# Kernel tuning notes

Measured on AMD Instinct MI355X. Metric: run time of the kernel, lower is better.

The kernel has to match this reference:

```python
import jax, jax.numpy as jnp
import numpy as np

EPS = 1e-15


def setup_inputs() -> dict:
    key = jax.random.key(0)
    ks = jax.random.split(key, 10)
    F, B, L = 10, 16384, 20          # num_field, batch, hist_len
    V, D = 1000000, 16               # sparse_feature_number, sparse_feature_dim
    FEAT, E, S, G, T = 160, 8, 64, 3, 32  # feature_size, expert_num, expert_size, gate_num, tower_size
    return {
        "ids": jax.random.randint(ks[0], (F, B, L), 0, V, dtype=jnp.int64),
        "emb_table": jax.random.uniform(ks[1], (V, D), jnp.float32, -1.0, 1.0),
        "expert_w": jax.random.normal(ks[2], (E, FEAT, S), jnp.float32) * 0.05,
        "expert_b": jnp.full((E, S), 0.1, jnp.float32),
        "gate_w": jax.random.normal(ks[3], (G, FEAT, E), jnp.float32) * 0.05,
        "gate_b": jnp.full((G, E), 0.1, jnp.float32),
        "tower_w": jax.random.normal(ks[4], (G, S, T), jnp.float32) * 0.05,
        "tower_b": jnp.full((G, T), 0.1, jnp.float32),
        "out_w": jax.random.normal(ks[5], (G, T, 2), jnp.float32) * 0.05,
        "out_b": jnp.full((G, 2), 0.1, jnp.float32),
    }


def reference(ids, emb_table, expert_w, expert_b, gate_w, gate_b,
              tower_w, tower_b, out_w, out_b):
    # Embedding lookup + sum over history: [F,B,L,D] -> [F,B,D]
    field_emb = emb_table[ids].sum(axis=2)
    B = field_emb.shape[1]
    # concat per-field embeddings along feature axis: [B, F*D]
    x = jnp.transpose(field_emb, (1, 0, 2)).reshape(B, -1)
    # all experts as one batched GEMM: [B,E,S]
    experts = jax.nn.relu(jnp.einsum('bf,efs->bes', x, expert_w) + expert_b)
    # gate softmax over experts: [B,G,E]
    gates = jax.nn.softmax(jnp.einsum('bf,gfe->bge', x, gate_w) + gate_b, axis=-1)
    # gate-weighted expert mixture: [B,G,S]
    mix = jnp.einsum('bge,bes->bgs', gates, experts)
    # towers: [B,G,T] -> logits [B,G,2]
    tow = jax.nn.relu(jnp.einsum('bgs,gst->bgt', mix, tower_w) + tower_b)
    logits = jnp.einsum('bgt,gto->bgo', tow, out_w) + out_b
    probs = jnp.clip(jax.nn.softmax(logits, axis=-1), EPS, 1.0 - EPS)  # [B,3,2]
    ctr, cvr, imp = probs[:, 0], probs[:, 1], probs[:, 2]
    ctr1 = ctr[:, 1:2]
    cvr1 = cvr[:, 1:2]
    ctcvr1 = ctr1 * cvr1
    ctcvr = jnp.concatenate([1.0 - ctcvr1, ctcvr1], axis=1)
    imp1 = imp[:, 1:2]
    # out_list packed along last axis: ctr(2), ctr1(1), cvr(2), cvr1(1), ctcvr(2), ctcvr1(1), imp1(1) -> [B,10]
    return jnp.concatenate([ctr, ctr1, cvr, cvr1, ctcvr, ctcvr1, imp1], axis=1)
```

## Files before the change

### kernel.cpp

```cpp
#include <hip/hip_runtime.h>
#include <hip/hip_bf16.h>
#include <cstdint>
#include <cstddef>

#define NFIELD 10
#define BATCH  16384
#define NIDS   20
#define DEMB   16
#define NFEAT  160
#define NEXP   8
#define NS     64
#define NG     3
#define NT     32

#define XB        ((size_t)BATCH * NFEAT * 2)
#define BP_OFF_B  XB
#define BM_OFF_B  (BP_OFF_B + 174080)
#define BT_OFF_B  (BM_OFF_B + 2176)
#define TB2_OFF_B (BT_OFF_B + 12288)
#define OWF_OFF_B (TB2_OFF_B + 384)
#define OBF_OFF_B (OWF_OFF_B + 768)
#define FLG_OFF_B (OBF_OFF_B + 32)

typedef short bfrag __attribute__((ext_vector_type(8)));
typedef float f32x4 __attribute__((ext_vector_type(4)));

__device__ __forceinline__ float bflo(uint32_t u) {
    union { uint32_t u; float f; } c; c.u = u << 16; return c.f;
}
__device__ __forceinline__ float bfhi(uint32_t u) {
    union { uint32_t u; float f; } c; c.u = u & 0xffff0000u; return c.f;
}
__device__ __forceinline__ float bf1(uint16_t v) {
    union { uint32_t u; float f; } c; c.u = ((uint32_t)v) << 16; return c.f;
}
__device__ __forceinline__ uint16_t f2bf(float f) {
    union { float f; uint32_t u; } c; c.f = f;
    uint32_t r = c.u + 0x7fffu + ((c.u >> 16) & 1u);
    return (uint16_t)(r >> 16);
}
__device__ __forceinline__ float ldw(const void* p, int i, bool bf) {
    return bf ? bf1(((const uint16_t*)p)[i]) : ((const float*)p)[i];
}
__device__ __forceinline__ uint16_t ldb16(const void* p, int i, bool bf) {
    return bf ? ((const uint16_t*)p)[i] : f2bf(((const float*)p)[i]);
}

__global__ __launch_bounds__(64) void sniff_dtypes(
    const uint32_t* __restrict__ ids_w,
    const uint32_t* __restrict__ emb_w,
    int* __restrict__ flags)
{
    int t = threadIdx.x;
    size_t p = (size_t)t * 25000;
    uint32_t hi = ids_w[2 * p + 1];
    int n_hi = __popcll(__ballot(hi != 0));

    size_t q = (size_t)t * 125000;
    uint32_t w = emb_w[q];
    uint32_t v = (w >> 8) & 0x7Fu;
    int n_bf = __popcll(__ballot(v >= 0x3Bu && v <= 0x3Fu));

    if (t == 0) {
        flags[0] = (n_hi < 8)   ? 1 : 0;
        flags[1] = (n_bf >= 32) ? 1 : 0;
    }
}

__global__ __launch_bounds__(256) void pack_weights(
    const void* __restrict__ ew, const void* __restrict__ eb,
    const void* __restrict__ gw, const void* __restrict__ gb,
    const void* __restrict__ tw, const void* __restrict__ tb,
    const void* __restrict__ ow, const void* __restrict__ ob,
    uint16_t* __restrict__ bp, float* __restrict__ bm,
    uint16_t* __restrict__ bt, float* __restrict__ tb2,
    float* __restrict__ owf, float* __restrict__ obf,
    const int* __restrict__ flags)
{
    const bool bf = flags[1] != 0;
    int i = blockIdx.x * 256 + threadIdx.x;
    if (i < 10880) {
        int nt = i / 320, rem = i % 320;
        int ks = rem / 64, l = rem % 64;
        int n  = nt * 16 + (l & 15);
        int kb = ks * 32 + ((l >> 4) * 8);
        uint16_t v[8];
        #pragma unroll
        for (int j = 0; j < 8; ++j) {
            int k = kb + j;
            uint16_t x;
            if (n < 512)      x = ldb16(ew, (n >> 6) * 10240 + k * 64 + (n & 63), bf);
            else if (n < 536) x = ldb16(gw, ((n - 512) >> 3) * 1280 + k * 8 + ((n - 512) & 7), bf);
            else              x = 0;
            v[j] = x;
        }
        uint4 o;
        o.x = (uint32_t)v[0] | ((uint32_t)v[1] << 16);
        o.y = (uint32_t)v[2] | ((uint32_t)v[3] << 16);
        o.z = (uint32_t)v[4] | ((uint32_t)v[5] << 16);
        o.w = (uint32_t)v[6] | ((uint32_t)v[7] << 16);
        ((uint4*)bp)[i] = o;
    } else if (i < 11648) {
        int it = i - 10880;
        int g = it / 256, rem = it % 256;
        int ntile = rem / 128, ks = (rem / 64) & 1, l = rem % 64;
        int t  = ntile * 16 + (l & 15);
        int sb = ks * 32 + ((l >> 4) * 8);
        uint16_t v[8];
        #pragma unroll
        for (int j = 0; j < 8; ++j)
            v[j] = ldb16(tw, g * 2048 + (sb + j) * 32 + t, bf);
        uint4 o;
        o.x = (uint32_t)v[0] | ((uint32_t)v[1] << 16);
        o.y = (uint32_t)v[2] | ((uint32_t)v[3] << 16);
        o.z = (uint32_t)v[4] | ((uint32_t)v[5] << 16);
        o.w = (uint32_t)v[6] | ((uint32_t)v[7] << 16);
        ((uint4*)bt)[it] = o;
    } else if (i < 12192) {
        int n = i - 11648;
        bm[n] = (n < 512) ? ldw(eb, n, bf) : (n < 536 ? ldw(gb, n - 512, bf) : 0.0f);
    } else if (i < 12288) {
        int n = i - 12192; tb2[n] = ldw(tb, n, bf);
    } else if (i < 12480) {
        int n = i - 12288; owf[n] = ldw(ow, n, bf);
    } else if (i < 12486) {
        int n = i - 12480; obf[n] = ldw(ob, n, bf);
    }
}

__global__ __launch_bounds__(256) void gather_sum(
    const void* __restrict__ ids_raw,
    const void* __restrict__ emb_raw,
    uint16_t* __restrict__ xout,
    const int* __restrict__ flags)
{
    const bool i64 = flags[0] != 0;
    const bool bf  = flags[1] != 0;
    int tid = blockIdx.x * 256 + threadIdx.x;
    int f = tid >> 14;
    int b = tid & (BATCH - 1);

    int idv[NIDS];
    if (i64) {
        const int4* p4 = (const int4*)((const long long*)ids_raw +
                                       ((size_t)f * BATCH + b) * NIDS);
        #pragma unroll
        for (int j = 0; j < NIDS / 2; ++j) {
            int4 q = p4[j];
            idv[2 * j + 0] = q.x;
            idv[2 * j + 1] = q.z;
        }
    } else {
        const int4* p4 = (const int4*)((const int*)ids_raw +
                                       ((size_t)f * BATCH + b) * NIDS);
        #pragma unroll
        for (int j = 0; j < NIDS / 4; ++j) {
            int4 q = p4[j];
            idv[4 * j + 0] = q.x; idv[4 * j + 1] = q.y;
            idv[4 * j + 2] = q.z; idv[4 * j + 3] = q.w;
        }
    }

    float acc[16];
    #pragma unroll
    for (int d = 0; d < 16; ++d) acc[d] = 0.0f;

    if (bf) {
        #pragma unroll 5
        for (int l = 0; l < NIDS; ++l) {
            const uint4* row = (const uint4*)((const uint16_t*)emb_raw +
                                              (size_t)idv[l] * DEMB);
            uint4 r0 = row[0];
            uint4 r1 = row[1];
            acc[0]  += bflo(r0.x); acc[1]  += bfhi(r0.x);
            acc[2]  += bflo(r0.y); acc[3]  += bfhi(r0.y);
            acc[4]  += bflo(r0.z); acc[5]  += bfhi(r0.z);
            acc[6]  += bflo(r0.w); acc[7]  += bfhi(r0.w);
            acc[8]  += bflo(r1.x); acc[9]  += bfhi(r1.x);
            acc[10] += bflo(r1.y); acc[11] += bfhi(r1.y);
            acc[12] += bflo(r1.z); acc[13] += bfhi(r1.z);
            acc[14] += bflo(r1.w); acc[15] += bfhi(r1.w);
        }
    } else {
        #pragma unroll 5
        for (int l = 0; l < NIDS; ++l) {
            const float4* row = (const float4*)((const float*)emb_raw +
                                                (size_t)idv[l] * DEMB);
            float4 r0 = row[0], r1 = row[1], r2 = row[2], r3 = row[3];
            acc[0]  += r0.x; acc[1]  += r0.y; acc[2]  += r0.z; acc[3]  += r0.w;
            acc[4]  += r1.x; acc[5]  += r1.y; acc[6]  += r1.z; acc[7]  += r1.w;
            acc[8]  += r2.x; acc[9]  += r2.y; acc[10] += r2.z; acc[11] += r2.w;
            acc[12] += r3.x; acc[13] += r3.y; acc[14] += r3.z; acc[15] += r3.w;
        }
    }

    uint32_t p[8];
    #pragma unroll
    for (int j = 0; j < 8; ++j)
        p[j] = (uint32_t)f2bf(acc[2 * j]) | ((uint32_t)f2bf(acc[2 * j + 1]) << 16);

    uint4* dst = (uint4*)(xout + (size_t)b * NFEAT + f * DEMB);
    dst[0] = make_uint4(p[0], p[1], p[2], p[3]);
    dst[1] = make_uint4(p[4], p[5], p[6], p[7]);
}

__global__ __launch_bounds__(256) void moe_fwd(
    const uint16_t* __restrict__ xbf,
    const uint16_t* __restrict__ bp,
    const float*    __restrict__ bm,
    const uint16_t* __restrict__ btw,
    const float*    __restrict__ btb,
    const float*    __restrict__ owf,
    const float*    __restrict__ obf,
    const void* __restrict__ ew,
    const void* __restrict__ eb,
    const void* __restrict__ gw,
    const void* __restrict__ gb,
    const void* __restrict__ tw,
    const void* __restrict__ tb,
    const int* __restrict__ flags,
    void* __restrict__ out)
{
    __shared__ uint16_t exp_lds[32][520];
    __shared__ float    gate_lds[32][33];
    __shared__ uint16_t mix_lds[32][200];
    __shared__ float    tow_lds[32][100];
    __shared__ float    prob_lds[32][6];
    __shared__ int      badf, badt;

    const bool bfw = flags[1] != 0;
    const int tid = threadIdx.x;
    const int w = tid >> 6, l = tid & 63;
    const int lm = l & 15, q = l >> 4;
    const int b0 = blockIdx.x * 32;
    const int mrow = (w & 1) * 16;
    const int nhalf = w >> 1;

    if (tid == 0) { badf = 0; badt = 0; }

    bfrag a[5];
    {
        const uint16_t* xr = xbf + (size_t)(b0 + mrow + lm) * NFEAT + q * 8;
        #pragma unroll
        for (int ks = 0; ks < 5; ++ks)
            a[ks] = *(const bfrag*)(xr + ks * 32);
    }

    const int nt0 = nhalf * 17;
    for (int it = 0; it < 17; ++it) {
        int nt = nt0 + it;
        f32x4 acc = {0.0f, 0.0f, 0.0f, 0.0f};
        const bfrag* bpp = (const bfrag*)bp + (size_t)(nt * 5) * 64 + l;
        #pragma unroll
        for (int ks = 0; ks < 5; ++ks) {
            bfrag b = bpp[ks * 64];
            acc = __builtin_amdgcn_mfma_f32_16x16x32_bf16(a[ks], b, acc, 0, 0, 0);
        }
        int col = nt * 16 + lm;
        float bias = bm[col];
        if (col < 512) {
            #pragma unroll
            for (int r = 0; r < 4; ++r)
                exp_lds[mrow + q * 4 + r][col] = f2bf(fmaxf(acc[r] + bias, 0.0f));
        } else {
            #pragma unroll
            for (int r = 0; r < 4; ++r)
                gate_lds[mrow + q * 4 + r][col - 512] = acc[r] + bias;
        }
    }
    __syncthreads();

    if (tid < 64) {
        int s = tid & 31;
        int c = (tid * 67) & 511;
        int e = c >> 6, ss = c & 63;
        const uint16_t* xr = xbf + (size_t)(b0 + s) * NFEAT;
        float acal = ldw(eb, c, bfw);
        for (int k = 0; k < NFEAT; ++k)
            acal = fmaf(bf1(xr[k]), ldw(ew, e * 10240 + k * 64 + ss, bfw), acal);
        float want = fmaxf(acal, 0.0f);
        float got  = bf1(exp_lds[s][c]);
        if (fabsf(want - got) > 0.06f + 0.01f * fabsf(want)) badf = 1;
    } else if (tid < 88) {
        int idx = tid - 64;
        int s   = (tid * 5) & 31;
        int g = idx >> 3, e = idx & 7;
        const uint16_t* xr = xbf + (size_t)(b0 + s) * NFEAT;
        float acal = ldw(gb, idx, bfw);
        for (int k = 0; k < NFEAT; ++k)
            acal = fmaf(bf1(xr[k]), ldw(gw, g * 1280 + k * 8 + e, bfw), acal);
        if (fabsf(acal - gate_lds[s][idx]) > 0.04f + 0.01f * fabsf(acal)) badf = 1;
    }
    __syncthreads();

    if (badf) {
        uint16_t* xs = &mix_lds[0][0];
        for (int i = tid; i < 32 * NFEAT; i += 256) {
            int s = i / NFEAT, k = i - s * NFEAT;
            xs[s * 200 + k] = xbf[(size_t)(b0 + s) * NFEAT + k];
        }
        __syncthreads();
        int s2 = tid >> 3, j2 = tid & 7;
        for (int c = j2; c < 512; c += 8) {
            int e = c >> 6, ss = c & 63;
            float acal = ldw(eb, c, bfw);
            #pragma unroll 4
            for (int k = 0; k < NFEAT; ++k)
                acal = fmaf(bf1(xs[s2 * 200 + k]), ldw(ew, e * 10240 + k * 64 + ss, bfw), acal);
            exp_lds[s2][c] = f2bf(fmaxf(acal, 0.0f));
        }
        if (j2 < 3) {
            int g = j2;
            for (int e = 0; e < 8; ++e) {
                float acal = ldw(gb, g * 8 + e, bfw);
                #pragma unroll 4
                for (int k = 0; k < NFEAT; ++k)
                    acal = fmaf(bf1(xs[s2 * 200 + k]), ldw(gw, g * 1280 + k * 8 + e, bfw), acal);
                gate_lds[s2][g * 8 + e] = acal;
            }
        }
        __syncthreads();
    }

    const int sm = tid >> 3, j = tid & 7;

    if (j < 3) {
        float* gl = &gate_lds[sm][j * 8];
        float m = gl[0];
        #pragma unroll
        for (int e = 1; e < 8; ++e) m = fmaxf(m, gl[e]);
        float ex[8], s = 0.0f;
        #pragma unroll
        for (int e = 0; e < 8; ++e) { ex[e] = __expf(gl[e] - m); s += ex[e]; }
        float inv = 1.0f / s;
        #pragma unroll
        for (int e = 0; e < 8; ++e) gl[e] = ex[e] * inv;
    }
    __syncthreads();

    for (int g = 0; g < NG; ++g) {
        float m8[8];
        #pragma unroll
        for (int i = 0; i < 8; ++i) m8[i] = 0.0f;
        #pragma unroll
        for (int e = 0; e < NEXP; ++e) {
            float gv = gate_lds[sm][g * 8 + e];
            uint4 u = *(const uint4*)&exp_lds[sm][e * 64 + j * 8];
            m8[0] = fmaf(gv, bflo(u.x), m8[0]); m8[1] = fmaf(gv, bfhi(u.x), m8[1]);
            m8[2] = fmaf(gv, bflo(u.y), m8[2]); m8[3] = fmaf(gv, bfhi(u.y), m8[3]);
            m8[4] = fmaf(gv, bflo(u.z), m8[4]); m8[5] = fmaf(gv, bfhi(u.z), m8[5]);
            m8[6] = fmaf(gv, bflo(u.w), m8[6]); m8[7] = fmaf(gv, bfhi(u.w), m8[7]);
        }
        uint4 o;
        o.x = (uint32_t)f2bf(m8[0]) | ((uint32_t)f2bf(m8[1]) << 16);
        o.y = (uint32_t)f2bf(m8[2]) | ((uint32_t)f2bf(m8[3]) << 16);
        o.z = (uint32_t)f2bf(m8[4]) | ((uint32_t)f2bf(m8[5]) << 16);
        o.w = (uint32_t)f2bf(m8[6]) | ((uint32_t)f2bf(m8[7]) << 16);
        *(uint4*)&mix_lds[sm][g * 64 + j * 8] = o;
    }
    __syncthreads();

    for (int u = w; u < 12; u += 4) {
        int g = u >> 2, mt = (u >> 1) & 1, ntile = u & 1;
        f32x4 acc = {0.0f, 0.0f, 0.0f, 0.0f};
        #pragma unroll
        for (int ks = 0; ks < 2; ++ks) {
            bfrag av = *(const bfrag*)&mix_lds[mt * 16 + lm][g * 64 + ks * 32 + q * 8];
            bfrag bv = *(const bfrag*)(btw + (size_t)((((g * 2 + ntile) * 2 + ks) * 64 + l)) * 8);
            acc = __builtin_amdgcn_mfma_f32_16x16x32_bf16(av, bv, acc, 0, 0, 0);
        }
        int t = ntile * 16 + lm;
        float bias = btb[g * 32 + t];
        #pragma unroll
        for (int r = 0; r < 4; ++r)
            tow_lds[mt * 16 + q * 4 + r][g * 32 + t] = fmaxf(acc[r] + bias, 0.0f);
    }
    __syncthreads();

    if (tid < 64) {
        int s   = tid & 31;
        int idx = (tid * 29) % 96;
        int g = idx >> 5, t = idx & 31;
        float acal = ldw(tb, g * 32 + t, bfw);
        for (int ss = 0; ss < NS; ++ss)
            acal = fmaf(bf1(mix_lds[s][g * 64 + ss]), ldw(tw, g * 2048 + ss * 32 + t, bfw), acal);
        float want = fmaxf(acal, 0.0f);
        if (fabsf(want - tow_lds[s][g * 32 + t]) > 0.04f + 0.01f * fabsf(want)) badt = 1;
    }
    __syncthreads();

    if (badt) {
        int s2 = tid >> 3, j2 = tid & 7;
        for (int idx = j2; idx < 96; idx += 8) {
            int g = idx >> 5, t = idx & 31;
            float acal = ldw(tb, g * 32 + t, bfw);
            #pragma unroll 4
            for (int ss = 0; ss < NS; ++ss)
                acal = fmaf(bf1(mix_lds[s2][g * 64 + ss]), ldw(tw, g * 2048 + ss * 32 + t, bfw), acal);
            tow_lds[s2][g * 32 + t] = fmaxf(acal, 0.0f);
        }
        __syncthreads();
    }

    if (j < 3) {
        int g = j;
        float l0 = obf[2 * g], l1 = obf[2 * g + 1];
        #pragma unroll 8
        for (int t = 0; t < NT; ++t) {
            float tv = tow_lds[sm][g * 32 + t];
            l0 = fmaf(tv, owf[g * 64 + 2 * t], l0);
            l1 = fmaf(tv, owf[g * 64 + 2 * t + 1], l1);
        }
        float m  = fmaxf(l0, l1);
        float e0 = __expf(l0 - m);
        float e1 = __expf(l1 - m);
        float inv = 1.0f / (e0 + e1);
        float p0 = fminf(fmaxf(e0 * inv, 1e-15f), 1.0f);
        float p1 = fminf(fmaxf(e1 * inv, 1e-15f), 1.0f);
        prob_lds[sm][2 * g + 0] = p0;
        prob_lds[sm][2 * g + 1] = p1;
    }
    __syncthreads();

    {
        float ctr0 = prob_lds[sm][0], ctr1 = prob_lds[sm][1];
        float cvr0 = prob_lds[sm][2], cvr1 = prob_lds[sm][3];
        float imp1 = prob_lds[sm][5];
        float ctcvr1 = ctr1 * cvr1;
        for (int o = j; o < 10; o += 8) {
            float v;
            switch (o) {
                case 0: v = ctr0; break;
                case 1: v = ctr1; break;
                case 2: v = ctr1; break;
                case 3: v = cvr0; break;
                case 4: v = cvr1; break;
                case 5: v = cvr1; break;
                case 6: v = 1.0f - ctcvr1; break;
                case 7: v = ctcvr1; break;
                case 8: v = ctcvr1; break;
                default: v = imp1; break;
            }
            if (bfw) ((uint16_t*)out)[(size_t)(b0 + sm) * 10 + o] = f2bf(v);
            else     ((float*)out)[(size_t)(b0 + sm) * 10 + o]    = v;
        }
    }
}

extern "C" void kernel_launch(void* const* d_in, const int* in_sizes, int n_in,
                              void* d_out, int out_size, void* d_ws, size_t ws_size,
                              hipStream_t stream) {
    const void* ids = d_in[0];
    const void* emb = d_in[1];

    char* ws = (char*)d_ws;
    uint16_t* xbf = (uint16_t*)ws;
    uint16_t* bpk = (uint16_t*)(ws + BP_OFF_B);
    float*    bm  = (float*)(ws + BM_OFF_B);
    uint16_t* btw = (uint16_t*)(ws + BT_OFF_B);
    float*    tb2 = (float*)(ws + TB2_OFF_B);
    float*    owf = (float*)(ws + OWF_OFF_B);
    float*    obf = (float*)(ws + OBF_OFF_B);
    int*    flags = (int*)(ws + FLG_OFF_B);

    sniff_dtypes<<<1, 64, 0, stream>>>((const uint32_t*)ids, (const uint32_t*)emb, flags);
    pack_weights<<<49, 256, 0, stream>>>(
        d_in[2], d_in[3], d_in[4], d_in[5], d_in[6], d_in[7], d_in[8], d_in[9],
        bpk, bm, btw, tb2, owf, obf, flags);
    gather_sum<<<(NFIELD * BATCH) / 256, 256, 0, stream>>>(ids, emb, xbf, flags);
    moe_fwd<<<BATCH / 32, 256, 0, stream>>>(
        xbf, bpk, bm, btw, tb2, owf, obf,
        d_in[2], d_in[3], d_in[4], d_in[5], d_in[6], d_in[7],
        flags, d_out);
}
```

Measured before the change: 209.5 us.

## Split embedding gather across two threads per row and drop MoE verification passes

The gather kernel now assigns two threads to each (field, batch) pair, each loading and summing half of the 16-dim embedding row. This doubles thread-level parallelism and the number of outstanding memory requests for the random-access gather, at the cost of loading the id list twice. The MoE kernel also drops its sampled scalar recomputation checks and fallback recompute paths for expert, gate and tower outputs, which removes serial per-thread dot products and extra barriers but also removes the safety net if the MFMA path were wrong.

```diff
diff --git a/kernel.cpp b/kernel.cpp
--- a/kernel.cpp
+++ b/kernel.cpp
@@ -137,8 +137,10 @@
     const bool i64 = flags[0] != 0;
     const bool bf  = flags[1] != 0;
     int tid = blockIdx.x * 256 + threadIdx.x;
-    int f = tid >> 14;
-    int b = tid & (BATCH - 1);
+    int h    = tid & 1;
+    int pair = tid >> 1;
+    int f = pair >> 14;
+    int b = pair & (BATCH - 1);
 
     int idv[NIDS];
     if (i64) {
@@ -161,47 +163,37 @@
         }
     }
 
-    float acc[16];
+    float acc[8];
     #pragma unroll
-    for (int d = 0; d < 16; ++d) acc[d] = 0.0f;
+    for (int d = 0; d < 8; ++d) acc[d] = 0.0f;
 
     if (bf) {
-        #pragma unroll 5
+        #pragma unroll
         for (int l = 0; l < NIDS; ++l) {
-            const uint4* row = (const uint4*)((const uint16_t*)emb_raw +
-                                              (size_t)idv[l] * DEMB);
-            uint4 r0 = row[0];
-            uint4 r1 = row[1];
-            acc[0]  += bflo(r0.x); acc[1]  += bfhi(r0.x);
-            acc[2]  += bflo(r0.y); acc[3]  += bfhi(r0.y);
-            acc[4]  += bflo(r0.z); acc[5]  += bfhi(r0.z);
-            acc[6]  += bflo(r0.w); acc[7]  += bfhi(r0.w);
-            acc[8]  += bflo(r1.x); acc[9]  += bfhi(r1.x);
-            acc[10] += bflo(r1.y); acc[11] += bfhi(r1.y);
-            acc[12] += bflo(r1.z); acc[13] += bfhi(r1.z);
-            acc[14] += bflo(r1.w); acc[15] += bfhi(r1.w);
+            uint4 r = *(const uint4*)((const uint16_t*)emb_raw +
+                                      (size_t)idv[l] * DEMB + h * 8);
+            acc[0] += bflo(r.x); acc[1] += bfhi(r.x);
+            acc[2] += bflo(r.y); acc[3] += bfhi(r.y);
+            acc[4] += bflo(r.z); acc[5] += bfhi(r.z);
+            acc[6] += bflo(r.w); acc[7] += bfhi(r.w);
         }
     } else {
-        #pragma unroll 5
+        #pragma unroll
         for (int l = 0; l < NIDS; ++l) {
-            const float4* row = (const float4*)((const float*)emb_raw +
-                                                (size_t)idv[l] * DEMB);
-            float4 r0 = row[0], r1 = row[1], r2 = row[2], r3 = row[3];
-            acc[0]  += r0.x; acc[1]  += r0.y; acc[2]  += r0.z; acc[3]  += r0.w;
-            acc[4]  += r1.x; acc[5]  += r1.y; acc[6]  += r1.z; acc[7]  += r1.w;
-            acc[8]  += r2.x; acc[9]  += r2.y; acc[10] += r2.z; acc[11] += r2.w;
-            acc[12] += r3.x; acc[13] += r3.y; acc[14] += r3.z; acc[15] += r3.w;
-        }
-    }
-
-    uint32_t p[8];
-    #pragma unroll
-    for (int j = 0; j < 8; ++j)
-        p[j] = (uint32_t)f2bf(acc[2 * j]) | ((uint32_t)f2bf(acc[2 * j + 1]) << 16);
-
-    uint4* dst = (uint4*)(xout + (size_t)b * NFEAT + f * DEMB);
-    dst[0] = make_uint4(p[0], p[1], p[2], p[3]);
-    dst[1] = make_uint4(p[4], p[5], p[6], p[7]);
+            const float4* p = (const float4*)((const float*)emb_raw +
+                                              (size_t)idv[l] * DEMB + h * 8);
+            float4 r0 = p[0], r1 = p[1];
+            acc[0] += r0.x; acc[1] += r0.y; acc[2] += r0.z; acc[3] += r0.w;
+            acc[4] += r1.x; acc[5] += r1.y; acc[6] += r1.z; acc[7] += r1.w;
+        }
+    }
+
+    uint4 o;
+    o.x = (uint32_t)f2bf(acc[0]) | ((uint32_t)f2bf(acc[1]) << 16);
+    o.y = (uint32_t)f2bf(acc[2]) | ((uint32_t)f2bf(acc[3]) << 16);
+    o.z = (uint32_t)f2bf(acc[4]) | ((uint32_t)f2bf(acc[5]) << 16);
+    o.w = (uint32_t)f2bf(acc[6]) | ((uint32_t)f2bf(acc[7]) << 16);
+    *(uint4*)(xout + (size_t)b * NFEAT + f * DEMB + h * 8) = o;
 }
 
 __global__ __launch_bounds__(256) void moe_fwd(
@@ -212,12 +204,6 @@
     const float*    __restrict__ btb,
     const float*    __restrict__ owf,
     const float*    __restrict__ obf,
-    const void* __restrict__ ew,
-    const void* __restrict__ eb,
-    const void* __restrict__ gw,
-    const void* __restrict__ gb,
-    const void* __restrict__ tw,
-    const void* __restrict__ tb,
     const int* __restrict__ flags,
     void* __restrict__ out)
 {
@@ -226,7 +212,6 @@
     __shared__ uint16_t mix_lds[32][200];
     __shared__ float    tow_lds[32][100];
     __shared__ float    prob_lds[32][6];
-    __shared__ int      badf, badt;
 
     const bool bfw = flags[1] != 0;
     const int tid = threadIdx.x;
@@ -235,8 +220,6 @@
     const int b0 = blockIdx.x * 32;
     const int mrow = (w & 1) * 16;
     const int nhalf = w >> 1;
-
-    if (tid == 0) { badf = 0; badt = 0; }
 
     bfrag a[5];
     {
@@ -270,58 +253,6 @@
     }
     __syncthreads();
 
-    if (tid < 64) {
-        int s = tid & 31;
-        int c = (tid * 67) & 511;
-        int e = c >> 6, ss = c & 63;
-        const uint16_t* xr = xbf + (size_t)(b0 + s) * NFEAT;
-        float acal = ldw(eb, c, bfw);
-        for (int k = 0; k < NFEAT; ++k)
-            acal = fmaf(bf1(xr[k]), ldw(ew, e * 10240 + k * 64 + ss, bfw), acal);
-        float want = fmaxf(acal, 0.0f);
-        float got  = bf1(exp_lds[s][c]);
-        if (fabsf(want - got) > 0.06f + 0.01f * fabsf(want)) badf = 1;
-    } else if (tid < 88) {
-        int idx = tid - 64;
-        int s   = (tid * 5) & 31;
-        int g = idx >> 3, e = idx & 7;
-        const uint16_t* xr = xbf + (size_t)(b0 + s) * NFEAT;
-        float acal = ldw(gb, idx, bfw);
-        for (int k = 0; k < NFEAT; ++k)
-            acal = fmaf(bf1(xr[k]), ldw(gw, g * 1280 + k * 8 + e, bfw), acal);
-        if (fabsf(acal - gate_lds[s][idx]) > 0.04f + 0.01f * fabsf(acal)) badf = 1;
-    }
-    __syncthreads();
-
-    if (badf) {
-        uint16_t* xs = &mix_lds[0][0];
-        for (int i = tid; i < 32 * NFEAT; i += 256) {
-            int s = i / NFEAT, k = i - s * NFEAT;
-            xs[s * 200 + k] = xbf[(size_t)(b0 + s) * NFEAT + k];
-        }
-        __syncthreads();
-        int s2 = tid >> 3, j2 = tid & 7;
-        for (int c = j2; c < 512; c += 8) {
-            int e = c >> 6, ss = c & 63;
-            float acal = ldw(eb, c, bfw);
-            #pragma unroll 4
-            for (int k = 0; k < NFEAT; ++k)
-                acal = fmaf(bf1(xs[s2 * 200 + k]), ldw(ew, e * 10240 + k * 64 + ss, bfw), acal);
-            exp_lds[s2][c] = f2bf(fmaxf(acal, 0.0f));
-        }
-        if (j2 < 3) {
-            int g = j2;
-            for (int e = 0; e < 8; ++e) {
-                float acal = ldw(gb, g * 8 + e, bfw);
-                #pragma unroll 4
-                for (int k = 0; k < NFEAT; ++k)
-                    acal = fmaf(bf1(xs[s2 * 200 + k]), ldw(gw, g * 1280 + k * 8 + e, bfw), acal);
-                gate_lds[s2][g * 8 + e] = acal;
-            }
-        }
-        __syncthreads();
-    }
-
     const int sm = tid >> 3, j = tid & 7;
 
     if (j < 3) {
@@ -376,31 +307,6 @@
             tow_lds[mt * 16 + q * 4 + r][g * 32 + t] = fmaxf(acc[r] + bias, 0.0f);
     }
     __syncthreads();
-
-    if (tid < 64) {
-        int s   = tid & 31;
-        int idx = (tid * 29) % 96;
-        int g = idx >> 5, t = idx & 31;
-        float acal = ldw(tb, g * 32 + t, bfw);
-        for (int ss = 0; ss < NS; ++ss)
-            acal = fmaf(bf1(mix_lds[s][g * 64 + ss]), ldw(tw, g * 2048 + ss * 32 + t, bfw), acal);
-        float want = fmaxf(acal, 0.0f);
-        if (fabsf(want - tow_lds[s][g * 32 + t]) > 0.04f + 0.01f * fabsf(want)) badt = 1;
-    }
-    __syncthreads();
-
-    if (badt) {
-        int s2 = tid >> 3, j2 = tid & 7;
-        for (int idx = j2; idx < 96; idx += 8) {
-            int g = idx >> 5, t = idx & 31;
-            float acal = ldw(tb, g * 32 + t, bfw);
-            #pragma unroll 4
-            for (int ss = 0; ss < NS; ++ss)
-                acal = fmaf(bf1(mix_lds[s2][g * 64 + ss]), ldw(tw, g * 2048 + ss * 32 + t, bfw), acal);
-            tow_lds[s2][g * 32 + t] = fmaxf(acal, 0.0f);
-        }
-        __syncthreads();
-    }
 
     if (j < 3) {
         int g = j;
@@ -467,9 +373,7 @@
     pack_weights<<<49, 256, 0, stream>>>(
         d_in[2], d_in[3], d_in[4], d_in[5], d_in[6], d_in[7], d_in[8], d_in[9],
         bpk, bm, btw, tb2, owf, obf, flags);
-    gather_sum<<<(NFIELD * BATCH) / 256, 256, 0, stream>>>(ids, emb, xbf, flags);
+    gather_sum<<<(NFIELD * BATCH * 2) / 256, 256, 0, stream>>>(ids, emb, xbf, flags);
     moe_fwd<<<BATCH / 32, 256, 0, stream>>>(
-        xbf, bpk, bm, btw, tb2, owf, obf,
-        d_in[2], d_in[3], d_in[4], d_in[5], d_in[6], d_in[7],
-        flags, d_out);
-}
+        xbf, bpk, bm, btw, tb2, owf, obf, flags, d_out);
+}
```

Measured after the change: 204.9 us. 2.2% less time.
